# Optimization experiments

Hardware: AMD Instinct MI355X
Metric: run time of the kernel (lower is better)

The kernel has to match this reference:

```python
import jax, jax.numpy as jnp
import numpy as np

D_MODEL = 1024
N_HEADS = 16
D_K = D_MODEL // N_HEADS
NEG = -1e10


def setup_inputs() -> dict:
    key = jax.random.key(0)
    ks = jax.random.split(key, 12)
    bs, sl = 2, 2048
    q = jax.random.normal(ks[0], (bs, sl, D_MODEL), dtype=jnp.float32)
    k = jax.random.normal(ks[1], (bs, sl, D_MODEL), dtype=jnp.float32)
    v = jax.random.normal(ks[2], (bs, sl, D_MODEL), dtype=jnp.float32)
    mask = jax.random.randint(ks[3], (bs, 1, sl, sl), 0, 2).astype(bool)
    s = 1.0 / np.sqrt(D_MODEL)
    Wq = jax.random.uniform(ks[4], (D_MODEL, D_MODEL), jnp.float32, -s, s)
    bq = jax.random.uniform(ks[5], (D_MODEL,), jnp.float32, -s, s)
    Wk = jax.random.uniform(ks[6], (D_MODEL, D_MODEL), jnp.float32, -s, s)
    bk = jax.random.uniform(ks[7], (D_MODEL,), jnp.float32, -s, s)
    Wv = jax.random.uniform(ks[8], (D_MODEL, D_MODEL), jnp.float32, -s, s)
    bv = jax.random.uniform(ks[9], (D_MODEL,), jnp.float32, -s, s)
    Wo = jax.random.uniform(ks[10], (D_MODEL, D_MODEL), jnp.float32, -s, s)
    bo = jax.random.uniform(ks[11], (D_MODEL,), jnp.float32, -s, s)
    return {"q": q, "k": k, "v": v, "mask": mask,
            "Wq": Wq, "bq": bq, "Wk": Wk, "bk": bk,
            "Wv": Wv, "bv": bv, "Wo": Wo, "bo": bo}


def reference(q, k, v, mask, Wq, bq, Wk, bk, Wv, bv, Wo, bo):
    bs, sl, _ = q.shape
    sl2 = k.shape[1]
    # linear projections (torch Linear: x @ W.T + b), split into heads: [b, h, s, d_k]
    qh = (q @ Wq.T + bq).reshape(bs, sl, N_HEADS, D_K).transpose(0, 2, 1, 3)
    kh = (k @ Wk.T + bk).reshape(bs, sl2, N_HEADS, D_K).transpose(0, 2, 1, 3)
    vh = (v @ Wv.T + bv).reshape(bs, sl2, N_HEADS, D_K).transpose(0, 2, 1, 3)
    scores = jnp.einsum('bhqd,bhkd->bhqk', qh, kh) / jnp.sqrt(jnp.float32(D_K))
    scores = jnp.where(mask, NEG, scores)
    attn = jax.nn.softmax(scores, axis=-1)
    z = jnp.einsum('bhqk,bhkd->bhqd', attn, vh)  # [b, h, sl, d_k]
    z = z.transpose(0, 2, 1, 3).reshape(bs, sl, D_MODEL)
    return z @ Wo.T + bo
```

## Files before the change

### kernel.cpp

```cpp
#include <hip/hip_runtime.h>

typedef __attribute__((ext_vector_type(8))) short short8;
typedef __attribute__((ext_vector_type(4))) float f32x4;
typedef __attribute__((ext_vector_type(16))) float f32x16;
typedef __attribute__((ext_vector_type(4))) unsigned int u32x4;

#define MFMA16(a, b, c) __builtin_amdgcn_mfma_f32_16x16x32_bf16((a), (b), (c), 0, 0, 0)
#define MFMA32(a, b, c) __builtin_amdgcn_mfma_f32_32x32x16_bf16((a), (b), (c), 0, 0, 0)

#if __has_builtin(__builtin_amdgcn_exp2f)
#define EXP2(x) __builtin_amdgcn_exp2f(x)
#else
#define EXP2(x) __expf((x) * 0.6931471805599453f)
#endif

__device__ __forceinline__ unsigned short f2bf(float f) {
  unsigned int u = __float_as_uint(f);
  u += 0x7FFFu + ((u >> 16) & 1u);
  return (unsigned short)(u >> 16);
}

__device__ __forceinline__ unsigned int cvtpk(float lo, float hi) {
  unsigned int r;
  asm("v_cvt_pk_bf16_f32 %0, %1, %2" : "=v"(r) : "v"(lo), "v"(hi));
  return r;
}

__device__ __forceinline__ short8 mk8(unsigned int a, unsigned int b,
                                      unsigned int c, unsigned int d) {
  u32x4 u = {a, b, c, d};
  return __builtin_bit_cast(short8, u);
}

__device__ __forceinline__ void gload16(const void* g, void* l) {
  __builtin_amdgcn_global_load_lds((const __attribute__((address_space(1))) void*)g,
                                   (__attribute__((address_space(3))) void*)l, 16, 0, 0);
}

__device__ __forceinline__ int swz(int row) {
  return (row & 7) ^ (((row >> 3) & 3) << 1);
}

__device__ __forceinline__ short8 fragld64(const unsigned short* base, int row, int kchunk) {
  int cc = kchunk ^ swz(row);
  return *(const short8*)(base + row * 64 + cc * 8);
}

__global__ void prep(const float* __restrict__ q, const float* __restrict__ k,
                     const float* __restrict__ v, const float* __restrict__ Wq,
                     const float* __restrict__ Wk, const float* __restrict__ Wv,
                     const float* __restrict__ Wo, const int* __restrict__ m,
                     unsigned short* __restrict__ xbf, unsigned short* __restrict__ wbf,
                     unsigned long long* __restrict__ mw) {
  const int bid = blockIdx.x, tid = threadIdx.x;
  if (bid >= 16384) {
    const int lane = tid & 63;
    const size_t wbase = ((size_t)(bid - 16384) * 4 + (tid >> 6)) * 4ull;
#pragma unroll
    for (int u = 0; u < 4; ++u) {
      size_t word = wbase + u;
      int x = m[word * 64 + lane];
      unsigned long long bb = __ballot(x != 0);
      if (lane == 0) mw[word] = bb;
    }
    return;
  }
  const float* src;
  unsigned short* dst;
  int i;
  if (bid < 12288) {
    int which = bid >> 12;
    i = (bid & 4095) * 256 + tid;
    src = (which == 0) ? q : ((which == 1) ? k : v);
    dst = xbf + (size_t)which * 4194304ull;
  } else {
    int which = (bid - 12288) >> 10;
    i = ((bid - 12288) & 1023) * 256 + tid;
    src = (which == 0) ? Wq : ((which == 1) ? Wk : ((which == 2) ? Wv : Wo));
    dst = wbf + (size_t)which * 1048576ull;
  }
  float4 vv = ((const float4*)src)[i];
  ushort4 o;
  o.x = f2bf(vv.x); o.y = f2bf(vv.y); o.z = f2bf(vv.z); o.w = f2bf(vv.w);
  ((ushort4*)dst)[i] = o;
}

template<bool OUT_BF16>
__global__ __launch_bounds__(256, 3) void gemm_bt(
    const unsigned short* __restrict__ Abase, const unsigned short* __restrict__ Bbase,
    const float* __restrict__ bias0, const float* __restrict__ bias1,
    const float* __restrict__ bias2, void* __restrict__ outv,
    unsigned short* __restrict__ vtgp, float scale0)
{
  constexpr int K = 1024, N = 1024;
  const int z = blockIdx.z;
  const unsigned short* A = Abase + (size_t)z * 4194304ull;
  const unsigned short* B = Bbase + (size_t)z * 1048576ull;
  const float* bias = (z == 0) ? bias0 : ((z == 1) ? bias1 : bias2);
  const float scale = (z == 0) ? scale0 : 1.0f;

  __shared__ unsigned short ldsA[128 * 64];
  __shared__ unsigned short ldsB[128 * 64];

  const int tid = threadIdx.x;
  const int lane = tid & 63, wid = tid >> 6;
  const int c16 = lane & 15, g = lane >> 4;
  const int m0 = blockIdx.y * 128, n0 = blockIdx.x * 128;
  const int wr = (wid >> 1) * 64, wc = (wid & 1) * 64;

  f32x4 acc[4][4] = {};

  for (int kt = 0; kt < K; kt += 64) {
    __syncthreads();
#pragma unroll
    for (int i = 0; i < 4; ++i) {
      int row = i * 32 + (tid >> 3);
      int cc = tid & 7;
      int scc = cc ^ swz(row);
      gload16(A + (size_t)(m0 + row) * K + kt + scc * 8, ldsA + row * 64 + cc * 8);
      gload16(B + (size_t)(n0 + row) * K + kt + scc * 8, ldsB + row * 64 + cc * 8);
    }
    __syncthreads();
#pragma unroll
    for (int kc = 0; kc < 2; ++kc) {
      short8 af[4], bf[4];
#pragma unroll
      for (int mi = 0; mi < 4; ++mi) af[mi] = fragld64(ldsA, wr + mi * 16 + c16, kc * 4 + g);
#pragma unroll
      for (int ni = 0; ni < 4; ++ni) bf[ni] = fragld64(ldsB, wc + ni * 16 + c16, kc * 4 + g);
#pragma unroll
      for (int mi = 0; mi < 4; ++mi)
#pragma unroll
        for (int ni = 0; ni < 4; ++ni)
          acc[mi][ni] = MFMA16(af[mi], bf[ni], acc[mi][ni]);
    }
  }

  if (OUT_BF16 && z == 2) {
#pragma unroll
    for (int mi = 0; mi < 4; ++mi)
#pragma unroll
      for (int ni = 0; ni < 4; ++ni) {
        int col = n0 + wc + ni * 16 + c16;
        float bb = bias[col];
        int row0 = m0 + wr + mi * 16 + g * 4;
        int b2 = row0 >> 11, s0 = row0 & 2047;
        int vrow = (b2 * 16 + (col >> 6)) * 64 + (col & 63);
        ushort4 o;
        o.x = f2bf(acc[mi][ni][0] + bb);
        o.y = f2bf(acc[mi][ni][1] + bb);
        o.z = f2bf(acc[mi][ni][2] + bb);
        o.w = f2bf(acc[mi][ni][3] + bb);
        *(ushort4*)(vtgp + (size_t)vrow * 2048 + s0) = o;
      }
    return;
  }

#pragma unroll
  for (int mi = 0; mi < 4; ++mi)
#pragma unroll
    for (int ni = 0; ni < 4; ++ni) {
      int col = n0 + wc + ni * 16 + c16;
      float bb = bias[col];
#pragma unroll
      for (int r = 0; r < 4; ++r) {
        int row = m0 + wr + mi * 16 + g * 4 + r;
        float v = (acc[mi][ni][r] + bb) * scale;
        if constexpr (OUT_BF16)
          ((unsigned short*)outv)[(size_t)z * 4194304ull + (size_t)row * N + col] = f2bf(v);
        else
          ((float*)outv)[(size_t)row * N + col] = v;
      }
    }
}

__device__ __forceinline__ void full_step(
    const unsigned short* __restrict__ kb, const unsigned short* __restrict__ vb,
    const short8 qf[4], unsigned long long mword, int ql, int hd,
    f32x16& z0, f32x16& z1, float& lrun)
{
  const unsigned int nbA = ((unsigned int)mword) >> (hd * 4);
  const unsigned int nbB = ((unsigned int)(mword >> 32)) >> (hd * 4);
  f32x16 sA, sB;
#pragma unroll
  for (int m = 0; m < 4; ++m) {
    unsigned int nA = (nbA >> (m * 8)) & 0xFu;
    unsigned int nB = (nbB >> (m * 8)) & 0xFu;
#pragma unroll
    for (int c = 0; c < 4; ++c) {
      sA[m * 4 + c] = ((nA >> c) & 1u) ? -1e10f : 0.0f;
      sB[m * 4 + c] = ((nB >> c) & 1u) ? -1e10f : 0.0f;
    }
  }
  __builtin_amdgcn_s_setprio(1);
#pragma unroll
  for (int kc = 0; kc < 4; ++kc) {
    short8 kfA = fragld64(kb, ql, kc * 2 + hd);
    short8 kfB = fragld64(kb, 32 + ql, kc * 2 + hd);
    sA = MFMA32(kfA, qf[kc], sA);
    sB = MFMA32(kfB, qf[kc], sB);
  }
  __builtin_amdgcn_s_setprio(0);
#pragma unroll
  for (int i = 0; i < 16; ++i) {
    sA[i] = EXP2(sA[i]);
    sB[i] = EXP2(sB[i]);
  }
  {
    float a0 = (sA[0] + sA[1]) + (sA[2] + sA[3]);
    float a1 = (sA[4] + sA[5]) + (sA[6] + sA[7]);
    float a2 = (sA[8] + sA[9]) + (sA[10] + sA[11]);
    float a3 = (sA[12] + sA[13]) + (sA[14] + sA[15]);
    float b0 = (sB[0] + sB[1]) + (sB[2] + sB[3]);
    float b1 = (sB[4] + sB[5]) + (sB[6] + sB[7]);
    float b2 = (sB[8] + sB[9]) + (sB[10] + sB[11]);
    float b3 = (sB[12] + sB[13]) + (sB[14] + sB[15]);
    lrun += ((a0 + a1) + (a2 + a3)) + ((b0 + b1) + (b2 + b3));
  }
  unsigned int wvA[8], wvB[8];
#pragma unroll
  for (int i = 0; i < 8; ++i) {
    wvA[i] = cvtpk(sA[2 * i], sA[2 * i + 1]);
    wvB[i] = cvtpk(sB[2 * i], sB[2 * i + 1]);
  }
#pragma unroll
  for (int m = 0; m < 2; ++m) {
    asm("v_permlane32_swap_b32 %0, %1" : "+v"(wvA[4 * m]), "+v"(wvA[4 * m + 2]));
    asm("v_permlane32_swap_b32 %0, %1" : "+v"(wvA[4 * m + 1]), "+v"(wvA[4 * m + 3]));
    asm("v_permlane32_swap_b32 %0, %1" : "+v"(wvB[4 * m]), "+v"(wvB[4 * m + 2]));
    asm("v_permlane32_swap_b32 %0, %1" : "+v"(wvB[4 * m + 1]), "+v"(wvB[4 * m + 3]));
  }
  __builtin_amdgcn_s_setprio(1);
  {
    short8 pfA0 = mk8(wvA[0], wvA[1], wvA[2], wvA[3]);
    short8 pfA1 = mk8(wvA[4], wvA[5], wvA[6], wvA[7]);
    short8 pfB0 = mk8(wvB[0], wvB[1], wvB[2], wvB[3]);
    short8 pfB1 = mk8(wvB[4], wvB[5], wvB[6], wvB[7]);
    z0 = MFMA32(pfA0, fragld64(vb, ql, 0 + hd), z0);
    z1 = MFMA32(pfA0, fragld64(vb, 32 + ql, 0 + hd), z1);
    z0 = MFMA32(pfA1, fragld64(vb, ql, 2 + hd), z0);
    z1 = MFMA32(pfA1, fragld64(vb, 32 + ql, 2 + hd), z1);
    z0 = MFMA32(pfB0, fragld64(vb, ql, 4 + hd), z0);
    z1 = MFMA32(pfB0, fragld64(vb, 32 + ql, 4 + hd), z1);
    z0 = MFMA32(pfB1, fragld64(vb, ql, 6 + hd), z0);
    z1 = MFMA32(pfB1, fragld64(vb, 32 + ql, 6 + hd), z1);
  }
  __builtin_amdgcn_s_setprio(0);
}

__global__ __launch_bounds__(256, 3) void attn(
    const unsigned short* __restrict__ qh, const unsigned short* __restrict__ kh,
    const unsigned short* __restrict__ vtg, const unsigned long long* __restrict__ mw,
    unsigned short* __restrict__ zbf)
{
  constexpr int SL = 2048, DM = 1024, NT = SL / 64;
  const int bid = blockIdx.x;
  const int g = bid & 31;
  const int qt = bid >> 5;
  const int h = g & 15, b = g >> 4;

  const int tid = threadIdx.x, lane = tid & 63, w = tid >> 6;
  const int ql = lane & 31, hd = lane >> 5;
  const int qa = qt * 128 + w * 32;

  __shared__ unsigned short kbuf[2][4096];
  __shared__ unsigned short vbuf[2][4096];

  short8 qf[4];
  {
    const size_t qrow = ((size_t)b * SL + qa + ql) * DM + (size_t)h * 64 + hd * 8;
#pragma unroll
    for (int kc = 0; kc < 4; ++kc)
      qf[kc] = *(const short8*)(qh + qrow + kc * 16);
  }

  f32x16 zacc0 = {}, zacc1 = {};
  float lrun = 0.f;

  const unsigned long long* mwq = mw + ((size_t)b * SL + qa + ql) * (SL / 64);
  unsigned long long mwc = mwq[0];

  const int kr = tid >> 3, cc = tid & 7;
  const int r0 = kr, r1 = kr + 32;
  const size_t kbase = (size_t)b * SL * DM + (size_t)h * 64;
  const size_t vbase = (size_t)((b * 16 + h) * 64) * (size_t)SL;
  const unsigned short* kp0 = kh + kbase + (size_t)r0 * DM + (cc ^ swz(r0)) * 8;
  const unsigned short* kp1 = kh + kbase + (size_t)r1 * DM + (cc ^ swz(r1)) * 8;
  const unsigned short* vp0 = vtg + vbase + (size_t)r0 * SL + (cc ^ swz(r0)) * 8;
  const unsigned short* vp1 = vtg + vbase + (size_t)r1 * SL + (cc ^ swz(r1)) * 8;

  gload16(kp0, kbuf[0] + r0 * 64 + cc * 8);
  gload16(kp1, kbuf[0] + r1 * 64 + cc * 8);
  gload16(vp0, vbuf[0] + r0 * 64 + cc * 8);
  gload16(vp1, vbuf[0] + r1 * 64 + cc * 8);

  for (int t = 0; t < NT; ++t) {
    const int cur = t & 1, nxt = cur ^ 1;
    __syncthreads();

    const bool more = (t + 1 < NT);
    unsigned long long mwn = 0;
    if (more) {
      kp0 += 64 * DM; kp1 += 64 * DM; vp0 += 64; vp1 += 64;
      gload16(kp0, kbuf[nxt] + r0 * 64 + cc * 8);
      gload16(kp1, kbuf[nxt] + r1 * 64 + cc * 8);
      gload16(vp0, vbuf[nxt] + r0 * 64 + cc * 8);
      gload16(vp1, vbuf[nxt] + r1 * 64 + cc * 8);
      mwn = mwq[t + 1];
    }

    full_step(kbuf[cur], vbuf[cur], qf, mwc, ql, hd, zacc0, zacc1, lrun);
    mwc = mwn;
  }

  lrun += __shfl_xor(lrun, 32);

  float invl = (lrun > 0.f) ? 1.f / lrun : 0.f;
#pragma unroll
  for (int reg = 0; reg < 16; ++reg) {
    int qrow = (reg & 3) + 8 * (reg >> 2) + 4 * hd;
    float il = __shfl(invl, qrow);
    size_t orow = ((size_t)b * SL + qa + qrow) * DM + (size_t)h * 64;
    zbf[orow + ql] = f2bf(zacc0[reg] * il);
    zbf[orow + 32 + ql] = f2bf(zacc1[reg] * il);
  }
}

extern "C" void kernel_launch(void* const* d_in, const int* in_sizes, int n_in,
                              void* d_out, int out_size, void* d_ws, size_t ws_size,
                              hipStream_t stream) {
  const float* q  = (const float*)d_in[0];
  const float* k  = (const float*)d_in[1];
  const float* v  = (const float*)d_in[2];
  const int* mask = (const int*)d_in[3];
  const float* Wq = (const float*)d_in[4];
  const float* bq = (const float*)d_in[5];
  const float* Wk = (const float*)d_in[6];
  const float* bk = (const float*)d_in[7];
  const float* Wv = (const float*)d_in[8];
  const float* bv = (const float*)d_in[9];
  const float* Wo = (const float*)d_in[10];
  const float* bo = (const float*)d_in[11];

  char* ws = (char*)d_ws;
  unsigned short* xbf = (unsigned short*)ws;
  unsigned short* zbf = (unsigned short*)(ws + 2097152);
  unsigned short* wbf = (unsigned short*)(ws + 25165824);
  unsigned short* qkv = (unsigned short*)(ws + 33554432);
  unsigned short* vtg = (unsigned short*)(ws + 58720256);
  unsigned long long* mwb = (unsigned long long*)d_out;

  prep<<<24576, 256, 0, stream>>>(q, k, v, Wq, Wk, Wv, Wo, mask, xbf, wbf, mwb);

  gemm_bt<true><<<dim3(8, 32, 3), 256, 0, stream>>>(xbf, wbf, bq, bk, bv, (void*)qkv,
                                                    vtg, 0.125f * 1.44269504088896f);
  attn<<<512, 256, 0, stream>>>(qkv, qkv + 4194304ull, vtg, mwb, zbf);
  gemm_bt<false><<<dim3(8, 32, 1), 256, 0, stream>>>(zbf, wbf + 3145728ull, bo, bo, bo,
                                                     d_out, nullptr, 1.0f);
}
```

Measured before the change: 139.3 us.

## Split attention key range across warp pairs and reduce partials in LDS

The attention kernel now gives each block 64 query rows instead of 128 and splits the 2048 keys between two warp pairs, each streaming 32-key tiles into its own double buffer. The two partial outputs and row sums are combined through shared memory at the end. The grid doubles to 1024 blocks and the occupancy hint rises to 4 blocks per CU, aiming for better CU fill and latency hiding. In exchange, each block loads K/V for fewer query rows, so K/V traffic per query roughly doubles, and it adds an extra reduction and barrier at the end.

```diff
diff --git a/kernel.cpp b/kernel.cpp
--- a/kernel.cpp
+++ b/kernel.cpp
@@ -44,6 +44,11 @@
 __device__ __forceinline__ short8 fragld64(const unsigned short* base, int row, int kchunk) {
   int cc = kchunk ^ swz(row);
   return *(const short8*)(base + row * 64 + cc * 8);
+}
+
+__device__ __forceinline__ short8 fragld32(const unsigned short* base, int row, int kchunk) {
+  int cc = kchunk ^ (swz(row) & 3);
+  return *(const short8*)(base + row * 32 + cc * 8);
 }
 
 __global__ void prep(const float* __restrict__ q, const float* __restrict__ k,
@@ -174,97 +179,71 @@
     }
 }
 
-__device__ __forceinline__ void full_step(
+__device__ __forceinline__ void step32(
     const unsigned short* __restrict__ kb, const unsigned short* __restrict__ vb,
-    const short8 qf[4], unsigned long long mword, int ql, int hd,
+    const short8 qf[4], unsigned int nb, int ql, int hd,
     f32x16& z0, f32x16& z1, float& lrun)
 {
-  const unsigned int nbA = ((unsigned int)mword) >> (hd * 4);
-  const unsigned int nbB = ((unsigned int)(mword >> 32)) >> (hd * 4);
-  f32x16 sA, sB;
+  const unsigned int nbs = nb >> (hd * 4);
+  f32x16 s;
 #pragma unroll
   for (int m = 0; m < 4; ++m) {
-    unsigned int nA = (nbA >> (m * 8)) & 0xFu;
-    unsigned int nB = (nbB >> (m * 8)) & 0xFu;
-#pragma unroll
-    for (int c = 0; c < 4; ++c) {
-      sA[m * 4 + c] = ((nA >> c) & 1u) ? -1e10f : 0.0f;
-      sB[m * 4 + c] = ((nB >> c) & 1u) ? -1e10f : 0.0f;
-    }
+    unsigned int nib = (nbs >> (m * 8)) & 0xFu;
+#pragma unroll
+    for (int c = 0; c < 4; ++c)
+      s[m * 4 + c] = ((nib >> c) & 1u) ? -1e10f : 0.0f;
   }
   __builtin_amdgcn_s_setprio(1);
 #pragma unroll
-  for (int kc = 0; kc < 4; ++kc) {
-    short8 kfA = fragld64(kb, ql, kc * 2 + hd);
-    short8 kfB = fragld64(kb, 32 + ql, kc * 2 + hd);
-    sA = MFMA32(kfA, qf[kc], sA);
-    sB = MFMA32(kfB, qf[kc], sB);
-  }
+  for (int kc = 0; kc < 4; ++kc)
+    s = MFMA32(fragld64(kb, ql, kc * 2 + hd), qf[kc], s);
   __builtin_amdgcn_s_setprio(0);
 #pragma unroll
-  for (int i = 0; i < 16; ++i) {
-    sA[i] = EXP2(sA[i]);
-    sB[i] = EXP2(sB[i]);
-  }
+  for (int i = 0; i < 16; ++i) s[i] = EXP2(s[i]);
   {
-    float a0 = (sA[0] + sA[1]) + (sA[2] + sA[3]);
-    float a1 = (sA[4] + sA[5]) + (sA[6] + sA[7]);
-    float a2 = (sA[8] + sA[9]) + (sA[10] + sA[11]);
-    float a3 = (sA[12] + sA[13]) + (sA[14] + sA[15]);
-    float b0 = (sB[0] + sB[1]) + (sB[2] + sB[3]);
-    float b1 = (sB[4] + sB[5]) + (sB[6] + sB[7]);
-    float b2 = (sB[8] + sB[9]) + (sB[10] + sB[11]);
-    float b3 = (sB[12] + sB[13]) + (sB[14] + sB[15]);
-    lrun += ((a0 + a1) + (a2 + a3)) + ((b0 + b1) + (b2 + b3));
-  }
-  unsigned int wvA[8], wvB[8];
-#pragma unroll
-  for (int i = 0; i < 8; ++i) {
-    wvA[i] = cvtpk(sA[2 * i], sA[2 * i + 1]);
-    wvB[i] = cvtpk(sB[2 * i], sB[2 * i + 1]);
-  }
-#pragma unroll
-  for (int m = 0; m < 2; ++m) {
-    asm("v_permlane32_swap_b32 %0, %1" : "+v"(wvA[4 * m]), "+v"(wvA[4 * m + 2]));
-    asm("v_permlane32_swap_b32 %0, %1" : "+v"(wvA[4 * m + 1]), "+v"(wvA[4 * m + 3]));
-    asm("v_permlane32_swap_b32 %0, %1" : "+v"(wvB[4 * m]), "+v"(wvB[4 * m + 2]));
-    asm("v_permlane32_swap_b32 %0, %1" : "+v"(wvB[4 * m + 1]), "+v"(wvB[4 * m + 3]));
-  }
+    float a0 = (s[0] + s[1]) + (s[2] + s[3]);
+    float a1 = (s[4] + s[5]) + (s[6] + s[7]);
+    float a2 = (s[8] + s[9]) + (s[10] + s[11]);
+    float a3 = (s[12] + s[13]) + (s[14] + s[15]);
+    lrun += (a0 + a1) + (a2 + a3);
+  }
+  unsigned int wv[8];
+#pragma unroll
+  for (int i = 0; i < 8; ++i) wv[i] = cvtpk(s[2 * i], s[2 * i + 1]);
+  asm("v_permlane32_swap_b32 %0, %1" : "+v"(wv[0]), "+v"(wv[2]));
+  asm("v_permlane32_swap_b32 %0, %1" : "+v"(wv[1]), "+v"(wv[3]));
+  asm("v_permlane32_swap_b32 %0, %1" : "+v"(wv[4]), "+v"(wv[6]));
+  asm("v_permlane32_swap_b32 %0, %1" : "+v"(wv[5]), "+v"(wv[7]));
   __builtin_amdgcn_s_setprio(1);
   {
-    short8 pfA0 = mk8(wvA[0], wvA[1], wvA[2], wvA[3]);
-    short8 pfA1 = mk8(wvA[4], wvA[5], wvA[6], wvA[7]);
-    short8 pfB0 = mk8(wvB[0], wvB[1], wvB[2], wvB[3]);
-    short8 pfB1 = mk8(wvB[4], wvB[5], wvB[6], wvB[7]);
-    z0 = MFMA32(pfA0, fragld64(vb, ql, 0 + hd), z0);
-    z1 = MFMA32(pfA0, fragld64(vb, 32 + ql, 0 + hd), z1);
-    z0 = MFMA32(pfA1, fragld64(vb, ql, 2 + hd), z0);
-    z1 = MFMA32(pfA1, fragld64(vb, 32 + ql, 2 + hd), z1);
-    z0 = MFMA32(pfB0, fragld64(vb, ql, 4 + hd), z0);
-    z1 = MFMA32(pfB0, fragld64(vb, 32 + ql, 4 + hd), z1);
-    z0 = MFMA32(pfB1, fragld64(vb, ql, 6 + hd), z0);
-    z1 = MFMA32(pfB1, fragld64(vb, 32 + ql, 6 + hd), z1);
+    short8 pf0 = mk8(wv[0], wv[1], wv[2], wv[3]);
+    short8 pf1 = mk8(wv[4], wv[5], wv[6], wv[7]);
+    z0 = MFMA32(pf0, fragld32(vb, ql, 0 + hd), z0);
+    z1 = MFMA32(pf0, fragld32(vb, 32 + ql, 0 + hd), z1);
+    z0 = MFMA32(pf1, fragld32(vb, ql, 2 + hd), z0);
+    z1 = MFMA32(pf1, fragld32(vb, 32 + ql, 2 + hd), z1);
   }
   __builtin_amdgcn_s_setprio(0);
 }
 
-__global__ __launch_bounds__(256, 3) void attn(
+__global__ __launch_bounds__(256, 4) void attn(
     const unsigned short* __restrict__ qh, const unsigned short* __restrict__ kh,
-    const unsigned short* __restrict__ vtg, const unsigned long long* __restrict__ mw,
+    const unsigned short* __restrict__ vtg, const unsigned int* __restrict__ mw,
     unsigned short* __restrict__ zbf)
 {
-  constexpr int SL = 2048, DM = 1024, NT = SL / 64;
+  constexpr int SL = 2048, DM = 1024, NSTEP = 32;
   const int bid = blockIdx.x;
   const int g = bid & 31;
   const int qt = bid >> 5;
   const int h = g & 15, b = g >> 4;
 
   const int tid = threadIdx.x, lane = tid & 63, w = tid >> 6;
+  const int qs = w & 1, hf = w >> 1;
   const int ql = lane & 31, hd = lane >> 5;
-  const int qa = qt * 128 + w * 32;
-
-  __shared__ unsigned short kbuf[2][4096];
-  __shared__ unsigned short vbuf[2][4096];
+  const int qa = qt * 64 + qs * 32;
+
+  __shared__ unsigned short kbuf[2][2][2048];
+  __shared__ unsigned short vbuf[2][2][2048];
 
   short8 qf[4];
   {
@@ -277,52 +256,73 @@
   f32x16 zacc0 = {}, zacc1 = {};
   float lrun = 0.f;
 
-  const unsigned long long* mwq = mw + ((size_t)b * SL + qa + ql) * (SL / 64);
-  unsigned long long mwc = mwq[0];
-
-  const int kr = tid >> 3, cc = tid & 7;
-  const int r0 = kr, r1 = kr + 32;
-  const size_t kbase = (size_t)b * SL * DM + (size_t)h * 64;
-  const size_t vbase = (size_t)((b * 16 + h) * 64) * (size_t)SL;
-  const unsigned short* kp0 = kh + kbase + (size_t)r0 * DM + (cc ^ swz(r0)) * 8;
-  const unsigned short* kp1 = kh + kbase + (size_t)r1 * DM + (cc ^ swz(r1)) * 8;
-  const unsigned short* vp0 = vtg + vbase + (size_t)r0 * SL + (cc ^ swz(r0)) * 8;
-  const unsigned short* vp1 = vtg + vbase + (size_t)r1 * SL + (cc ^ swz(r1)) * 8;
-
-  gload16(kp0, kbuf[0] + r0 * 64 + cc * 8);
-  gload16(kp1, kbuf[0] + r1 * 64 + cc * 8);
-  gload16(vp0, vbuf[0] + r0 * 64 + cc * 8);
-  gload16(vp1, vbuf[0] + r1 * 64 + cc * 8);
-
-  for (int t = 0; t < NT; ++t) {
+  const unsigned int* mwq = mw + ((size_t)b * SL + qa + ql) * 64 + hf * 32;
+  unsigned int mwc = mwq[0];
+
+  const int lw = (tid >> 6) & 1;
+  const int krow = lw * 16 + (lane >> 3), kcc = lane & 7;
+  const int vrow = lw * 32 + (lane >> 2), vcc = lane & 3;
+  const size_t kbase = (size_t)b * SL * DM + (size_t)h * 64 + (size_t)(hf * 1024) * DM;
+  const size_t vbase = (size_t)((b * 16 + h) * 64) * (size_t)SL + hf * 1024;
+  const unsigned short* kp1 = kh + kbase + (size_t)krow * DM + ((kcc ^ swz(krow)) * 8);
+  const unsigned short* kp2 = kh + kbase + (size_t)(krow + 8) * DM + ((kcc ^ swz(krow + 8)) * 8);
+  const unsigned short* vp1 = vtg + vbase + (size_t)vrow * SL + ((vcc ^ (swz(vrow) & 3)) * 8);
+  const unsigned short* vp2 = vtg + vbase + (size_t)(vrow + 16) * SL + ((vcc ^ (swz(vrow + 16) & 3)) * 8);
+
+  gload16(kp1, kbuf[hf][0] + krow * 64 + kcc * 8);
+  gload16(kp2, kbuf[hf][0] + (krow + 8) * 64 + kcc * 8);
+  gload16(vp1, vbuf[hf][0] + vrow * 32 + vcc * 8);
+  gload16(vp2, vbuf[hf][0] + (vrow + 16) * 32 + vcc * 8);
+
+  for (int t = 0; t < NSTEP; ++t) {
     const int cur = t & 1, nxt = cur ^ 1;
     __syncthreads();
 
-    const bool more = (t + 1 < NT);
-    unsigned long long mwn = 0;
+    const bool more = (t + 1 < NSTEP);
+    unsigned int mwn = 0;
     if (more) {
-      kp0 += 64 * DM; kp1 += 64 * DM; vp0 += 64; vp1 += 64;
-      gload16(kp0, kbuf[nxt] + r0 * 64 + cc * 8);
-      gload16(kp1, kbuf[nxt] + r1 * 64 + cc * 8);
-      gload16(vp0, vbuf[nxt] + r0 * 64 + cc * 8);
-      gload16(vp1, vbuf[nxt] + r1 * 64 + cc * 8);
+      kp1 += 32 * DM; kp2 += 32 * DM; vp1 += 32; vp2 += 32;
+      gload16(kp1, kbuf[hf][nxt] + krow * 64 + kcc * 8);
+      gload16(kp2, kbuf[hf][nxt] + (krow + 8) * 64 + kcc * 8);
+      gload16(vp1, vbuf[hf][nxt] + vrow * 32 + vcc * 8);
+      gload16(vp2, vbuf[hf][nxt] + (vrow + 16) * 32 + vcc * 8);
       mwn = mwq[t + 1];
     }
 
-    full_step(kbuf[cur], vbuf[cur], qf, mwc, ql, hd, zacc0, zacc1, lrun);
+    step32(kbuf[hf][cur], vbuf[hf][cur], qf, mwc, ql, hd, zacc0, zacc1, lrun);
     mwc = mwn;
   }
 
   lrun += __shfl_xor(lrun, 32);
 
-  float invl = (lrun > 0.f) ? 1.f / lrun : 0.f;
-#pragma unroll
-  for (int reg = 0; reg < 16; ++reg) {
-    int qrow = (reg & 3) + 8 * (reg >> 2) + 4 * hd;
-    float il = __shfl(invl, qrow);
-    size_t orow = ((size_t)b * SL + qa + qrow) * DM + (size_t)h * 64;
-    zbf[orow + ql] = f2bf(zacc0[reg] * il);
-    zbf[orow + 32 + ql] = f2bf(zacc1[reg] * il);
+  __syncthreads();
+  float* zsh = (float*)&kbuf[0][0][0];
+  float* lsh = (float*)&vbuf[0][0][0];
+  if (hf == 1) {
+#pragma unroll
+    for (int i = 0; i < 16; ++i) {
+      zsh[i * 128 + qs * 64 + lane] = zacc0[i];
+      zsh[(16 + i) * 128 + qs * 64 + lane] = zacc1[i];
+    }
+    if (lane < 32) lsh[qs * 32 + ql] = lrun;
+  }
+  __syncthreads();
+  if (hf == 0) {
+#pragma unroll
+    for (int i = 0; i < 16; ++i) {
+      zacc0[i] += zsh[i * 128 + qs * 64 + lane];
+      zacc1[i] += zsh[(16 + i) * 128 + qs * 64 + lane];
+    }
+    lrun += lsh[qs * 32 + ql];
+    float invl = (lrun > 0.f) ? 1.f / lrun : 0.f;
+#pragma unroll
+    for (int reg = 0; reg < 16; ++reg) {
+      int qrow = (reg & 3) + 8 * (reg >> 2) + 4 * hd;
+      float il = __shfl(invl, qrow);
+      size_t orow = ((size_t)b * SL + qa + qrow) * DM + (size_t)h * 64;
+      zbf[orow + ql] = f2bf(zacc0[reg] * il);
+      zbf[orow + 32 + ql] = f2bf(zacc1[reg] * il);
+    }
   }
 }
 
@@ -354,7 +354,7 @@
 
   gemm_bt<true><<<dim3(8, 32, 3), 256, 0, stream>>>(xbf, wbf, bq, bk, bv, (void*)qkv,
                                                     vtg, 0.125f * 1.44269504088896f);
-  attn<<<512, 256, 0, stream>>>(qkv, qkv + 4194304ull, vtg, mwb, zbf);
+  attn<<<1024, 256, 0, stream>>>(qkv, qkv + 4194304ull, vtg, (const unsigned int*)mwb, zbf);
   gemm_bt<false><<<dim3(8, 32, 1), 256, 0, stream>>>(zbf, wbf + 3145728ull, bo, bo, bo,
                                                      d_out, nullptr, 1.0f);
 }
```

New measurement: 146.3 us. 5.1% more time.
